# Kernel tuning notes

Hardware: AMD Instinct MI355X
Metric: run time of the kernel (lower is better)

The kernel has to match this reference:

```python
import jax, jax.numpy as jnp
import numpy as np


def setup_inputs() -> dict:
    key = jax.random.key(0)
    B, C, H, W = 32, 1024, 32, 32
    K = 256
    corr = jax.random.normal(key, (B, C, H, W), dtype=jnp.float32)
    select_indices = jnp.arange(K, dtype=jnp.int64)
    return {"corr": corr, "select_indices": select_indices}


def reference(corr, select_indices):
    # corr: [B, C, H, W]
    max_corr = jnp.max(corr, axis=1, keepdims=True)    # [B,1,H,W]
    avg_corr = jnp.mean(corr, axis=1, keepdims=True)   # [B,1,H,W]
    # per-channel total response: sum over spatial dims -> [B, C]
    value = jnp.sum(corr, axis=(2, 3))
    # descending sort indices along channel dim, then keep selected ranks
    sort_v_idx = jnp.argsort(-value, axis=1)           # [B, C]
    sel_idx = sort_v_idx[:, select_indices]            # [B, K]
    # batched gather of the selected channels (vectorized, no python loop)
    sort_corr = jnp.take_along_axis(corr, sel_idx[:, :, None, None], axis=1)  # [B,K,H,W]
    return jnp.concatenate([max_corr, avg_corr, sort_corr], axis=1)  # [B, 2+K, H, W]
```

## Files before the change

kernel.cpp:

```cpp
#include <hip/hip_runtime.h>
#include <hip/hip_bf16.h>


#define BB  32
#define CC  1024
#define HW  1024
#define NCH 32
#define CPC 32

__global__ __launch_bounds__(256)
void k_pass1(const float* __restrict__ corr,
             float* __restrict__ pmax,
             float* __restrict__ psum,
             double* __restrict__ value) {
    __shared__ double lds[CPC * 4];
    const int tid  = threadIdx.x;
    const int lane = tid & 63;
    const int wid  = tid >> 6;
    const int b  = blockIdx.x / NCH;
    const int cc = blockIdx.x % NCH;

    const float4* base = (const float4*)(corr + (((size_t)b * CC) + (size_t)cc * CPC) * HW);

    float4 vmax = make_float4(-__builtin_inff(), -__builtin_inff(),
                              -__builtin_inff(), -__builtin_inff());
    float4 vsum = make_float4(0.f, 0.f, 0.f, 0.f);

    #pragma unroll 4
    for (int c = 0; c < CPC; ++c) {
        float4 x = base[(size_t)c * (HW / 4) + tid];
        vmax.x = fmaxf(vmax.x, x.x); vmax.y = fmaxf(vmax.y, x.y);
        vmax.z = fmaxf(vmax.z, x.z); vmax.w = fmaxf(vmax.w, x.w);
        vsum.x += x.x; vsum.y += x.y; vsum.z += x.z; vsum.w += x.w;

        double s = ((double)x.x + (double)x.y) + ((double)x.z + (double)x.w);
        #pragma unroll
        for (int off = 32; off >= 1; off >>= 1)
            s += __shfl_down(s, off);
        if (lane == 0) lds[c * 4 + wid] = s;
    }
    __syncthreads();
    if (tid < CPC) {
        const double v = (lds[tid * 4 + 0] + lds[tid * 4 + 1])
                       + (lds[tid * 4 + 2] + lds[tid * 4 + 3]);
        value[(size_t)b * CC + (size_t)cc * CPC + tid] = v;
    }

    const size_t o = ((size_t)blockIdx.x * HW) + (size_t)tid * 4;
    *(float4*)(pmax + o) = vmax;
    *(float4*)(psum + o) = vsum;
}

__global__ __launch_bounds__(256)
void k_pass2(const float* __restrict__ pmax,
             const float* __restrict__ psum,
             float* __restrict__ out) {
    const int gid = blockIdx.x * 256 + threadIdx.x;
    const int b  = gid >> 10;
    const int hw = gid & (HW - 1);
    float m = -__builtin_inff();
    float s = 0.f;
    #pragma unroll 8
    for (int cc = 0; cc < NCH; ++cc) {
        const size_t o = (((size_t)b * NCH + cc) << 10) + hw;
        m = fmaxf(m, pmax[o]);
        s += psum[o];
    }
    const size_t ob = (size_t)b * (2 + 256) * HW;
    out[ob + hw]      = m;
    out[ob + HW + hw] = s * (1.0f / 1024.0f);
}

__global__ __launch_bounds__(64)
void k_rank(const double* __restrict__ value, int* __restrict__ sorted, int K) {
    __shared__ double vs[CC];
    const int b     = blockIdx.x >> 4;
    const int chunk = blockIdx.x & 15;
    const int tid   = threadIdx.x;

    for (int i = tid; i < CC; i += 64)
        vs[i] = value[(size_t)b * CC + i];
    __syncthreads();

    const int    c  = chunk * 64 + tid;
    const double my = vs[c];
    int rank = 0;
    #pragma unroll 8
    for (int j = 0; j < CC; ++j) {
        const double vj = vs[j];
        rank += (vj > my) || (vj == my && j < c) ? 1 : 0;
    }
    if (rank < K)
        sorted[(size_t)b * CC + rank] = c;
}

__global__ __launch_bounds__(256)
void k_gather(const float* __restrict__ corr,
              const int* __restrict__ sorted,
              const int* __restrict__ selidx,
              float* __restrict__ out, int K) {
    const int b = blockIdx.x / K;
    const int k = blockIdx.x % K;
    int ks = selidx[k];
    ks = min(max(ks, 0), CC - 1);
    int c = sorted[(size_t)b * CC + ks];
    c = min(max(c, 0), CC - 1);

    const float4* src = (const float4*)(corr + (((size_t)b * CC) + c) * HW);
    float4*       dst = (float4*)(out + (((size_t)b * (2 + 256)) + 2 + k) * HW);
    dst[threadIdx.x] = src[threadIdx.x];
}

extern "C" void kernel_launch(void* const* d_in, const int* in_sizes, int n_in,
                              void* d_out, int out_size, void* d_ws, size_t ws_size,
                              hipStream_t stream) {
    const float* corr = (const float*)d_in[0];
    const int*   sel  = (const int*)d_in[1];
    float*       out  = (float*)d_out;

    const int K = out_size / (BB * HW) - 2;

    float*  pmax   = (float*)d_ws;
    float*  psum   = pmax + (size_t)BB * NCH * HW;
    double* value  = (double*)(psum + (size_t)BB * NCH * HW);
    int*    sorted = (int*)(value + (size_t)BB * CC);

    k_pass1<<<BB * NCH, 256, 0, stream>>>(corr, pmax, psum, value);
    k_pass2<<<(BB * HW) / 256, 256, 0, stream>>>(pmax, psum, out);
    k_rank<<<BB * 16, 64, 0, stream>>>(value, sorted, K);
    k_gather<<<BB * K, 256, 0, stream>>>(corr, sorted, sel, out, K);
}
```

Measured before the change: 245.3 us.

## Give each wave whole channels in pass1 and split rank comparisons across four lanes

In pass1 each wavefront now reads whole channels of 8 per wave with 4 float4 loads per lane. Per-channel sums are reduced within a single wave and written straight out, which removes the per-channel LDS write and block barrier. Per-position max and sum partials from the four waves are merged through LDS once at the end. The rank kernel moves from 64 to 256 threads per block, with four lanes sharing each channel's comparison loop and combining counts by shuffle, plus LDS padding. This adds parallelism to the latency-bound rank step at the cost of a little more LDS and an extra barrier.

```diff
diff --git a/kernel.cpp b/kernel.cpp
--- a/kernel.cpp
+++ b/kernel.cpp
@@ -13,42 +13,66 @@
              float* __restrict__ pmax,
              float* __restrict__ psum,
              double* __restrict__ value) {
-    __shared__ double lds[CPC * 4];
+    __shared__ float4 lmax[4][4][64];
+    __shared__ float4 lsum[4][4][64];
     const int tid  = threadIdx.x;
     const int lane = tid & 63;
-    const int wid  = tid >> 6;
-    const int b  = blockIdx.x / NCH;
-    const int cc = blockIdx.x % NCH;
+    const int w    = tid >> 6;
+    const int b    = blockIdx.x / NCH;
+    const int cc   = blockIdx.x % NCH;
 
-    const float4* base = (const float4*)(corr + (((size_t)b * CC) + (size_t)cc * CPC) * HW);
+    const float4* cbase = (const float4*)(corr + (((size_t)b * CC) + (size_t)cc * CPC) * HW);
 
-    float4 vmax = make_float4(-__builtin_inff(), -__builtin_inff(),
+    float4 vmax[4], vsum[4];
+    #pragma unroll
+    for (int k = 0; k < 4; ++k) {
+        vmax[k] = make_float4(-__builtin_inff(), -__builtin_inff(),
                               -__builtin_inff(), -__builtin_inff());
-    float4 vsum = make_float4(0.f, 0.f, 0.f, 0.f);
+        vsum[k] = make_float4(0.f, 0.f, 0.f, 0.f);
+    }
 
-    #pragma unroll 4
-    for (int c = 0; c < CPC; ++c) {
-        float4 x = base[(size_t)c * (HW / 4) + tid];
-        vmax.x = fmaxf(vmax.x, x.x); vmax.y = fmaxf(vmax.y, x.y);
-        vmax.z = fmaxf(vmax.z, x.z); vmax.w = fmaxf(vmax.w, x.w);
-        vsum.x += x.x; vsum.y += x.y; vsum.z += x.z; vsum.w += x.w;
+    #pragma unroll 2
+    for (int i = 0; i < 8; ++i) {
+        const int cl = w * 8 + i;
+        const float4* ch = cbase + (size_t)cl * (HW / 4);
+        float4 x[4];
+        #pragma unroll
+        for (int k = 0; k < 4; ++k) x[k] = ch[lane + 64 * k];
 
-        double s = ((double)x.x + (double)x.y) + ((double)x.z + (double)x.w);
+        double s = 0.0;
+        #pragma unroll
+        for (int k = 0; k < 4; ++k) {
+            vmax[k].x = fmaxf(vmax[k].x, x[k].x); vmax[k].y = fmaxf(vmax[k].y, x[k].y);
+            vmax[k].z = fmaxf(vmax[k].z, x[k].z); vmax[k].w = fmaxf(vmax[k].w, x[k].w);
+            vsum[k].x += x[k].x; vsum[k].y += x[k].y;
+            vsum[k].z += x[k].z; vsum[k].w += x[k].w;
+            s += ((double)x[k].x + (double)x[k].y) + ((double)x[k].z + (double)x[k].w);
+        }
         #pragma unroll
         for (int off = 32; off >= 1; off >>= 1)
             s += __shfl_down(s, off);
-        if (lane == 0) lds[c * 4 + wid] = s;
-    }
-    __syncthreads();
-    if (tid < CPC) {
-        const double v = (lds[tid * 4 + 0] + lds[tid * 4 + 1])
-                       + (lds[tid * 4 + 2] + lds[tid * 4 + 3]);
-        value[(size_t)b * CC + (size_t)cc * CPC + tid] = v;
+        if (lane == 0)
+            value[(size_t)b * CC + (size_t)cc * CPC + cl] = s;
     }
 
-    const size_t o = ((size_t)blockIdx.x * HW) + (size_t)tid * 4;
-    *(float4*)(pmax + o) = vmax;
-    *(float4*)(psum + o) = vsum;
+    #pragma unroll
+    for (int k = 0; k < 4; ++k) { lmax[w][k][lane] = vmax[k]; lsum[w][k][lane] = vsum[k]; }
+    __syncthreads();
+
+    {
+        const int k  = tid >> 6, ln = tid & 63;
+        float4 m = lmax[0][k][ln], s = lsum[0][k][ln];
+        #pragma unroll
+        for (int ww = 1; ww < 4; ++ww) {
+            float4 a = lmax[ww][k][ln], d = lsum[ww][k][ln];
+            m.x = fmaxf(m.x, a.x); m.y = fmaxf(m.y, a.y);
+            m.z = fmaxf(m.z, a.z); m.w = fmaxf(m.w, a.w);
+            s.x += d.x; s.y += d.y; s.z += d.z; s.w += d.w;
+        }
+        const size_t o = ((size_t)blockIdx.x * (HW / 4)) + tid;
+        ((float4*)pmax)[o] = m;
+        ((float4*)psum)[o] = s;
+    }
 }
 
 __global__ __launch_bounds__(256)
@@ -71,27 +95,32 @@
     out[ob + HW + hw] = s * (1.0f / 1024.0f);
 }
 
-__global__ __launch_bounds__(64)
+__global__ __launch_bounds__(256)
 void k_rank(const double* __restrict__ value, int* __restrict__ sorted, int K) {
-    __shared__ double vs[CC];
+    __shared__ double vs[CC + 4];
     const int b     = blockIdx.x >> 4;
     const int chunk = blockIdx.x & 15;
     const int tid   = threadIdx.x;
 
-    for (int i = tid; i < CC; i += 64)
-        vs[i] = value[(size_t)b * CC + i];
+    for (int i = tid; i < CC; i += 256)
+        vs[i + (i >> 8)] = value[(size_t)b * CC + i];
     __syncthreads();
 
-    const int    c  = chunk * 64 + tid;
-    const double my = vs[c];
-    int rank = 0;
+    const int    c    = chunk * 64 + (tid >> 2);
+    const int    jq   = tid & 3;
+    const double my   = vs[c + (c >> 8)];
+    const int    jb   = jq * 257;
+    const int    j0   = jq * 256;
+    int r = 0;
     #pragma unroll 8
-    for (int j = 0; j < CC; ++j) {
-        const double vj = vs[j];
-        rank += (vj > my) || (vj == my && j < c) ? 1 : 0;
+    for (int j = 0; j < 256; ++j) {
+        const double vj = vs[jb + j];
+        r += (vj > my) || (vj == my && (j0 + j) < c) ? 1 : 0;
     }
-    if (rank < K)
-        sorted[(size_t)b * CC + rank] = c;
+    r += __shfl_down(r, 2);
+    r += __shfl_down(r, 1);
+    if (jq == 0 && r < K)
+        sorted[(size_t)b * CC + r] = c;
 }
 
 __global__ __launch_bounds__(256)
@@ -127,6 +156,6 @@
 
     k_pass1<<<BB * NCH, 256, 0, stream>>>(corr, pmax, psum, value);
     k_pass2<<<(BB * HW) / 256, 256, 0, stream>>>(pmax, psum, out);
-    k_rank<<<BB * 16, 64, 0, stream>>>(value, sorted, K);
+    k_rank<<<BB * 16, 256, 0, stream>>>(value, sorted, K);
     k_gather<<<BB * K, 256, 0, stream>>>(corr, sorted, sel, out, K);
 }
```

Result: faster. 231.2 us (-5.7%).
